# Kernel tuning notes

Hardware: AMD Instinct MI355X
Metric: run time of the kernel (lower is better)

## Reference

```python
import jax, jax.numpy as jnp
import numpy as np

N_PER_GRAPH = 32
DEGREE = 8
N_GRAPHS = 2048
IN_CH = 64
HID = 64
OUT = 4
EPS = 1e-5


def setup_inputs() -> dict:
    key = jax.random.key(0)
    ks = jax.random.split(key, 12)
    N = N_GRAPHS * N_PER_GRAPH
    # ring connectivity: node i -> (i+d) mod 32 within each graph, d=1..DEGREE
    i = np.arange(N_PER_GRAPH)
    offs = np.arange(1, DEGREE + 1)
    s = np.repeat(i, DEGREE)
    d = (s + np.tile(offs, N_PER_GRAPH)) % N_PER_GRAPH
    base = (np.arange(N_GRAPHS) * N_PER_GRAPH)[:, None]
    src = (base + s[None, :]).reshape(-1)
    dst = (base + d[None, :]).reshape(-1)
    edge_index = jnp.asarray(np.stack([src, dst]).astype(np.int32))
    batch = jnp.asarray((np.arange(N) // N_PER_GRAPH).astype(np.int32))

    def w(k, shape, fan_in):
        return jax.random.normal(k, shape, jnp.float32) / np.float32(np.sqrt(fan_in))

    return dict(
        x=jax.random.normal(ks[0], (N, IN_CH), jnp.float32),
        edge_weight=jax.random.uniform(ks[1], (edge_index.shape[1],), jnp.float32),
        W1a=w(ks[2], (IN_CH, HID), IN_CH), W1b=w(ks[3], (IN_CH, HID), IN_CH),
        b1=jnp.zeros((HID,), jnp.float32), g1=jnp.ones((HID,), jnp.float32), be1=jnp.zeros((HID,), jnp.float32),
        W2a=w(ks[4], (HID, 2 * HID), HID), W2b=w(ks[5], (HID, 2 * HID), HID),
        b2=jnp.zeros((2 * HID,), jnp.float32), g2=jnp.ones((2 * HID,), jnp.float32), be2=jnp.zeros((2 * HID,), jnp.float32),
        W3a=w(ks[6], (2 * HID, 2 * HID), 2 * HID), W3b=w(ks[7], (2 * HID, 2 * HID), 2 * HID),
        b3=jnp.zeros((2 * HID,), jnp.float32), g3=jnp.ones((2 * HID,), jnp.float32), be3=jnp.zeros((2 * HID,), jnp.float32),
        fcW=w(ks[8], (2 * HID, OUT), 2 * HID), fcb=jnp.zeros((OUT,), jnp.float32),
        edge_index=edge_index, batch=batch,
    )


def cheb_conv(x, src, dst, ew, W0, W1, b):
    # PyG ChebConv, K=2, sym normalization, lambda_max=2:
    # scaled Laplacian L_hat = L - I = -D^{-1/2} A D^{-1/2} (diag exactly 0)
    n = x.shape[0]
    deg = jnp.zeros((n,), x.dtype).at[src].add(ew)
    dinv = jnp.where(deg > 0, jax.lax.rsqrt(deg), 0.0)
    norm = -dinv[src] * ew * dinv[dst]
    tx1 = jnp.zeros_like(x).at[dst].add(norm[:, None] * x[src])  # [n, C] gather-scatter
    return x @ W0 + tx1 @ W1 + b


def batch_norm(x, g, b):
    # training-mode BatchNorm over the node dimension (biased variance, as torch)
    m = x.mean(0)
    v = x.var(0)
    return (x - m) * jax.lax.rsqrt(v + EPS) * g + b


def pool_half(x, src, dst, ew):
    # deterministic stand-in for graclus: pair consecutive nodes (pairs stay
    # within a graph since each graph has an even node count).
    n = x.shape[0]
    cluster = jnp.arange(n) // 2
    x2 = jax.ops.segment_max(x, cluster, num_segments=n // 2)
    s2, d2 = src // 2, dst // 2
    # zero-weight self loops == removing them (contribute 0 to degree & messages);
    # keeping duplicate edges == coalescing with sum under segment_sum ops.
    ew2 = jnp.where(s2 == d2, jnp.zeros_like(ew), ew)
    return x2, s2, d2, ew2


def forward(x, edge_weight, W1a, W1b, b1, g1, be1, W2a, W2b, b2, g2, be2,
            W3a, W3b, b3, g3, be3, fcW, fcb, edge_index, batch):
    src, dst = edge_index[0], edge_index[1]
    ew = edge_weight
    h = jax.nn.softplus(batch_norm(cheb_conv(x, src, dst, ew, W1a, W1b, b1), g1, be1))
    h, src, dst, ew = pool_half(h, src, dst, ew)
    h = jax.nn.softplus(batch_norm(cheb_conv(h, src, dst, ew, W2a, W2b, b2), g2, be2))
    h, src, dst, ew = pool_half(h, src, dst, ew)
    h = jax.nn.softplus(batch_norm(cheb_conv(h, src, dst, ew, W3a, W3b, b3), g3, be3))
    batch3 = batch[::4]  # batch vector after two halvings of consecutive pairs
    sums = jax.ops.segment_sum(h, batch3, num_segments=N_GRAPHS)
    cnt = jax.ops.segment_sum(jnp.ones((h.shape[0],), h.dtype), batch3, num_segments=N_GRAPHS)
    hg = sums / jnp.maximum(cnt, 1.0)[:, None]
    return jax.nn.log_softmax(hg @ fcW + fcb, axis=1)


def reference(x, edge_weight, W1a, W1b, b1, g1, be1, W2a, W2b, b2, g2, be2,
              W3a, W3b, b3, g3, be3, fcW, fcb, edge_index, batch):
    return forward(x, edge_weight, W1a, W1b, b1, g1, be1, W2a, W2b, b2, g2, be2,
                   W3a, W3b, b3, g3, be3, fcW, fcb, edge_index, batch)
```

## Files before the change

kernel.cpp:

```cpp
#include <hip/hip_runtime.h>

#define EPSV 1e-5f

typedef __attribute__((ext_vector_type(8))) short short8;
typedef __attribute__((ext_vector_type(4))) float f32x4;

__device__ __forceinline__ float softplus_f(float x){
    return fmaxf(x, 0.f) + log1pf(expf(-fabsf(x)));
}
__device__ __forceinline__ float bf2f(short u){
    union{unsigned int i; float f;} x; x.i = ((unsigned int)(unsigned short)u) << 16; return x.f;
}
__device__ __forceinline__ short f2bf(float f){
    union{float f; unsigned int i;} x; x.f = f;
    unsigned int r = x.i + 0x7fffu + ((x.i >> 16) & 1u);
    return (short)(r >> 16);
}

#define W1TA_OFF 0
#define W1TB_OFF 4608
#define W2TA_OFF 9216
#define W2TB_OFF 18432
#define W3TA_OFF 27648
#define W3TB_OFF 45056
#define WT_TOTAL 62464

__global__ void k_prep(const float* __restrict__ W1a, const float* __restrict__ W1b,
                       const float* __restrict__ W2a, const float* __restrict__ W2b,
                       const float* __restrict__ W3a, const float* __restrict__ W3b,
                       short* __restrict__ wt){
    int blk = blockIdx.x, tid = threadIdx.x;
    const float* src; short* dst; int N, SP, base;
    if      (blk < 16){  src = W1a; dst = wt + W1TA_OFF; N = 64;  SP = 72;  base = blk; }
    else if (blk < 32){  src = W1b; dst = wt + W1TB_OFF; N = 64;  SP = 72;  base = blk - 16; }
    else if (blk < 64){  src = W2a; dst = wt + W2TA_OFF; N = 128; SP = 72;  base = blk - 32; }
    else if (blk < 96){  src = W2b; dst = wt + W2TB_OFF; N = 128; SP = 72;  base = blk - 64; }
    else if (blk < 160){ src = W3a; dst = wt + W3TA_OFF; N = 128; SP = 136; base = blk - 96; }
    else              {  src = W3b; dst = wt + W3TB_OFF; N = 128; SP = 136; base = blk - 160; }
    int e = base * 256 + tid;
    int k = e / N, c = e % N;
    dst[c * SP + k] = f2bf(src[e]);
}

__global__ __launch_bounds__(256) void k_gat1(const float* __restrict__ x, const float* __restrict__ ew,
        short* __restrict__ xb1, short* __restrict__ tx1){
    __shared__ float ews[256], nrm[256], dinv[32];
    __shared__ __align__(16) short xsb[32][72];
    int g = blockIdx.x, tid = threadIdx.x;
    ews[tid] = ew[(size_t)g*256 + tid];
    {   const float4* xg = (const float4*)(x + (size_t)g*32*64);
        #pragma unroll
        for (int p = 0; p < 2; ++p){
            int i4 = tid + p*256;
            int r = i4 >> 4, cc = (i4 & 15)*4;
            float4 v = xg[i4];
            xsb[r][cc+0] = f2bf(v.x); xsb[r][cc+1] = f2bf(v.y);
            xsb[r][cc+2] = f2bf(v.z); xsb[r][cc+3] = f2bf(v.w);
        }
    }
    __syncthreads();
    if (tid < 32){
        float d = 0.f;
        #pragma unroll
        for (int k = 0; k < 8; ++k) d += ews[tid*8 + k];
        dinv[tid] = d > 0.f ? rsqrtf(d) : 0.f;
    }
    __syncthreads();
    {   int se = tid >> 3, de = (se + (tid & 7) + 1) & 31;
        nrm[tid] = -dinv[se] * ews[tid] * dinv[de]; }
    __syncthreads();
    int v = tid >> 3, ch = (tid & 7)*8;
    *(short8*)&xb1[((size_t)g*32 + v)*64 + ch] = *(const short8*)&xsb[v][ch];
    float acc[8];
    #pragma unroll
    for (int j = 0; j < 8; ++j) acc[j] = 0.f;
    #pragma unroll
    for (int k = 0; k < 8; ++k){
        int sl = (v - k - 1) & 31;
        float nw = nrm[sl*8 + k];
        short8 xv = *(const short8*)&xsb[sl][ch];
        #pragma unroll
        for (int j = 0; j < 8; ++j) acc[j] = fmaf(nw, bf2f(xv[j]), acc[j]);
    }
    short8 o;
    #pragma unroll
    for (int j = 0; j < 8; ++j) o[j] = f2bf(acc[j]);
    *(short8*)&tx1[((size_t)g*32 + v)*64 + ch] = o;
}

__global__ __launch_bounds__(256) void k_gat2(const short* __restrict__ h1, const float* __restrict__ ew,
        const float* __restrict__ scl1, const float* __restrict__ sft1,
        short* __restrict__ xb2, short* __restrict__ tx2){
    __shared__ float ews[256], nrm[256], dinv[16];
    __shared__ float scl[64], sft[64];
    __shared__ __align__(16) short xpb[16][72];
    int g = blockIdx.x, tid = threadIdx.x;
    ews[tid] = ew[(size_t)g*256 + tid];
    if (tid < 64){ scl[tid] = scl1[tid]; sft[tid] = sft1[tid]; }
    __syncthreads();
    if (tid < 128){
        int vo = tid >> 3, ch = (tid & 7)*8;
        short8 a = *(const short8*)&h1[((size_t)g*32 + 2*vo)*64 + ch];
        short8 b = *(const short8*)&h1[((size_t)g*32 + 2*vo + 1)*64 + ch];
        short8 o;
        #pragma unroll
        for (int j = 0; j < 8; ++j){
            float s = scl[ch+j], t = sft[ch+j];
            float va = softplus_f(bf2f(a[j])*s + t);
            float vb = softplus_f(bf2f(b[j])*s + t);
            o[j] = f2bf(fmaxf(va, vb));
        }
        *(short8*)&xpb[vo][ch] = o;
        *(short8*)&xb2[((size_t)g*16 + vo)*64 + ch] = o;
    }
    if (tid < 16){
        float d = 0.f;
        for (int t = tid*16; t < tid*16 + 16; ++t){
            int se = t >> 3, de = (se + (t & 7) + 1) & 31;
            float wv = ((se >> 1) == (de >> 1)) ? 0.f : ews[t];
            d += wv;
        }
        dinv[tid] = d > 0.f ? rsqrtf(d) : 0.f;
    }
    __syncthreads();
    {   int se = tid >> 3, de = (se + (tid & 7) + 1) & 31;
        float wv = ((se >> 1) == (de >> 1)) ? 0.f : ews[tid];
        nrm[tid] = -dinv[se >> 1] * wv * dinv[de >> 1]; }
    __syncthreads();
    if (tid < 128){
        int v = tid >> 3, ch = (tid & 7)*8;
        float acc[8];
        #pragma unroll
        for (int j = 0; j < 8; ++j) acc[j] = 0.f;
        #pragma unroll
        for (int dd = 0; dd < 2; ++dd){
            int d = v*2 + dd;
            #pragma unroll
            for (int k = 0; k < 8; ++k){
                int sl = (d - k - 1) & 31;
                float nw = nrm[sl*8 + k];
                short8 xv = *(const short8*)&xpb[sl >> 1][ch];
                #pragma unroll
                for (int j = 0; j < 8; ++j) acc[j] = fmaf(nw, bf2f(xv[j]), acc[j]);
            }
        }
        short8 o;
        #pragma unroll
        for (int j = 0; j < 8; ++j) o[j] = f2bf(acc[j]);
        *(short8*)&tx2[((size_t)g*16 + v)*64 + ch] = o;
    }
}

__global__ __launch_bounds__(256) void k_gat3(const short* __restrict__ h2, const float* __restrict__ ew,
        const float* __restrict__ scl2, const float* __restrict__ sft2,
        short* __restrict__ xb3, short* __restrict__ tx3){
    __shared__ float ews[256], nrm[256], dinv[8];
    __shared__ float scl[128], sft[128];
    __shared__ __align__(16) short xpb[8][136];
    int g = blockIdx.x, tid = threadIdx.x;
    ews[tid] = ew[(size_t)g*256 + tid];
    if (tid < 128){ scl[tid] = scl2[tid]; sft[tid] = sft2[tid]; }
    __syncthreads();
    if (tid < 128){
        int vo = tid >> 4, ch = (tid & 15)*8;
        short8 a = *(const short8*)&h2[((size_t)g*16 + 2*vo)*128 + ch];
        short8 b = *(const short8*)&h2[((size_t)g*16 + 2*vo + 1)*128 + ch];
        short8 o;
        #pragma unroll
        for (int j = 0; j < 8; ++j){
            float s = scl[ch+j], t = sft[ch+j];
            float va = softplus_f(bf2f(a[j])*s + t);
            float vb = softplus_f(bf2f(b[j])*s + t);
            o[j] = f2bf(fmaxf(va, vb));
        }
        *(short8*)&xpb[vo][ch] = o;
        *(short8*)&xb3[((size_t)g*8 + vo)*128 + ch] = o;
    }
    if (tid < 8){
        float d = 0.f;
        for (int t = tid*32; t < tid*32 + 32; ++t){
            int se = t >> 3, de = (se + (t & 7) + 1) & 31;
            float wv = ((se >> 2) == (de >> 2)) ? 0.f : ews[t];
            d += wv;
        }
        dinv[tid] = d > 0.f ? rsqrtf(d) : 0.f;
    }
    __syncthreads();
    {   int se = tid >> 3, de = (se + (tid & 7) + 1) & 31;
        float wv = ((se >> 2) == (de >> 2)) ? 0.f : ews[tid];
        nrm[tid] = -dinv[se >> 2] * wv * dinv[de >> 2]; }
    __syncthreads();
    if (tid < 128){
        int v = tid >> 4, ch = (tid & 15)*8;
        float acc[8];
        #pragma unroll
        for (int j = 0; j < 8; ++j) acc[j] = 0.f;
        #pragma unroll
        for (int dd = 0; dd < 4; ++dd){
            int d = v*4 + dd;
            #pragma unroll
            for (int k = 0; k < 8; ++k){
                int sl = (d - k - 1) & 31;
                float nw = nrm[sl*8 + k];
                short8 xv = *(const short8*)&xpb[sl >> 2][ch];
                #pragma unroll
                for (int j = 0; j < 8; ++j) acc[j] = fmaf(nw, bf2f(xv[j]), acc[j]);
            }
        }
        short8 o;
        #pragma unroll
        for (int j = 0; j < 8; ++j) o[j] = f2bf(acc[j]);
        *(short8*)&tx3[((size_t)g*8 + v)*128 + ch] = o;
    }
}

template<int BM, int CIN, int COUT, int NB>
__global__ __launch_bounds__(256) void k_gemm(const short* __restrict__ xb, const short* __restrict__ tx,
        const short* __restrict__ Wa, const short* __restrict__ Wb, int WSP,
        const float* __restrict__ bias, short* __restrict__ h, float* __restrict__ P){
    constexpr int RPW = BM/4, RT = RPW/16, CT = COUT/16, KC = CIN/64;
    __shared__ __align__(16) short As[BM][72];
    __shared__ __align__(16) short Bs[COUT][72];
    __shared__ float ssum[COUT], ssq[COUT];
    int blk = blockIdx.x, tid = threadIdx.x;
    int lane = tid & 63, w = tid >> 6, lrow = lane & 15, lk8 = lane >> 4;
    if (tid < COUT){ ssum[tid] = 0.f; ssq[tid] = 0.f; }
    f32x4 acc[RT][CT];
    #pragma unroll
    for (int rt = 0; rt < RT; ++rt)
        #pragma unroll
        for (int ct = 0; ct < CT; ++ct) acc[rt][ct] = (f32x4){0,0,0,0};

    #pragma unroll
    for (int seg = 0; seg < 2; ++seg){
        const short* Ag = seg ? tx : xb;
        const short* Wg = seg ? Wb : Wa;
        #pragma unroll
        for (int kc = 0; kc < KC; ++kc){
            __syncthreads();
            for (int idx = tid; idx < BM*8; idx += 256){
                int r = idx >> 3, ko = (idx & 7)*8;
                *(short8*)&As[r][ko] =
                    *(const short8*)&Ag[((size_t)(blk*BM + r))*CIN + kc*64 + ko];
            }
            for (int idx = tid; idx < COUT*8; idx += 256){
                int c = idx >> 3, ko = (idx & 7)*8;
                *(short8*)&Bs[c][ko] =
                    *(const short8*)&Wg[(size_t)c*WSP + kc*64 + ko];
            }
            __syncthreads();
            #pragma unroll
            for (int ks = 0; ks < 2; ++ks){
                short8 af[RT];
                #pragma unroll
                for (int rt = 0; rt < RT; ++rt)
                    af[rt] = *(const short8*)&As[w*RPW + rt*16 + lrow][ks*32 + lk8*8];
                #pragma unroll
                for (int ct = 0; ct < CT; ++ct){
                    short8 bf = *(const short8*)&Bs[ct*16 + lrow][ks*32 + lk8*8];
                    #pragma unroll
                    for (int rt = 0; rt < RT; ++rt)
                        acc[rt][ct] = __builtin_amdgcn_mfma_f32_16x16x32_bf16(af[rt], bf, acc[rt][ct], 0, 0, 0);
                }
            }
        }
    }
    #pragma unroll
    for (int ct = 0; ct < CT; ++ct){
        int col = ct*16 + lrow;
        float bb = bias[col];
        float s = 0.f, q = 0.f;
        #pragma unroll
        for (int rt = 0; rt < RT; ++rt){
            #pragma unroll
            for (int e = 0; e < 4; ++e){
                float v = acc[rt][ct][e] + bb;
                int row = blk*BM + w*RPW + rt*16 + lk8*4 + e;
                h[(size_t)row*COUT + col] = f2bf(v);
                s += v; q += v*v;
            }
        }
        s += __shfl_xor(s, 16); s += __shfl_xor(s, 32);
        q += __shfl_xor(q, 16); q += __shfl_xor(q, 32);
        if (lane < 16){ atomicAdd(&ssum[col], s); atomicAdd(&ssq[col], q); }
    }
    __syncthreads();
    if (tid < COUT){
        P[(size_t)tid*NB + blk]          = ssum[tid];
        P[(size_t)(COUT + tid)*NB + blk] = ssq[tid];
    }
}

template<int C, int NB>
__global__ void k_red(const float* __restrict__ P, const float* __restrict__ gamma,
                      const float* __restrict__ beta, float nl_inv,
                      float* __restrict__ scl, float* __restrict__ sft){
    __shared__ float r1[128], r2[128];
    int c = blockIdx.x, t = threadIdx.x;
    if (t < 128){
        float s = 0.f;
        for (int i = t; i < NB; i += 128) s += P[(size_t)c*NB + i];
        r1[t] = s;
    } else {
        float q = 0.f;
        for (int i = t - 128; i < NB; i += 128) q += P[(size_t)(C + c)*NB + i];
        r2[t - 128] = q;
    }
    __syncthreads();
    for (int s = 64; s > 0; s >>= 1){
        if (t < s) r1[t] += r1[t + s];
        else if (t >= 128 && t - 128 < s) r2[t - 128] += r2[t - 128 + s];
        __syncthreads();
    }
    if (t == 0){
        float m = r1[0] * nl_inv;
        float var = r2[0] * nl_inv - m*m;
        float rs = rsqrtf(var + EPSV) * gamma[c];
        scl[c] = rs;
        sft[c] = beta[c] - m*rs;
    }
}

__global__ __launch_bounds__(256) void k_head(const short* __restrict__ h3,
        const float* __restrict__ scl3, const float* __restrict__ sft3,
        const float* __restrict__ fcW, const float* __restrict__ fcb,
        float* __restrict__ out){
    int tid = threadIdx.x, w = tid >> 6, lane = tid & 63;
    int g = blockIdx.x*4 + w;
    int c0 = lane*2;
    float sc0 = scl3[c0], sh0 = sft3[c0];
    float sc1 = scl3[c0+1], sh1 = sft3[c0+1];
    float acc0 = 0.f, acc1 = 0.f;
    #pragma unroll
    for (int n = 0; n < 8; ++n){
        unsigned int v = *(const unsigned int*)&h3[((size_t)g*8 + n)*128 + c0];
        union{unsigned int i; float f;} lo, hi;
        lo.i = v << 16; hi.i = v & 0xffff0000u;
        acc0 += softplus_f(lo.f*sc0 + sh0);
        acc1 += softplus_f(hi.f*sc1 + sh1);
    }
    float hg0 = acc0 * 0.125f, hg1 = acc1 * 0.125f;
    float4 w0 = ((const float4*)fcW)[c0];
    float4 w1 = ((const float4*)fcW)[c0+1];
    float z0 = hg0*w0.x + hg1*w1.x;
    float z1 = hg0*w0.y + hg1*w1.y;
    float z2 = hg0*w0.z + hg1*w1.z;
    float z3 = hg0*w0.w + hg1*w1.w;
    #pragma unroll
    for (int d = 1; d < 64; d <<= 1){
        z0 += __shfl_xor(z0, d); z1 += __shfl_xor(z1, d);
        z2 += __shfl_xor(z2, d); z3 += __shfl_xor(z3, d);
    }
    if (lane == 0){
        z0 += fcb[0]; z1 += fcb[1]; z2 += fcb[2]; z3 += fcb[3];
        float mx = fmaxf(fmaxf(z0, z1), fmaxf(z2, z3));
        float lse = mx + logf(expf(z0-mx) + expf(z1-mx) + expf(z2-mx) + expf(z3-mx));
        *(float4*)(out + (size_t)g*4) = make_float4(z0-lse, z1-lse, z2-lse, z3-lse);
    }
}

extern "C" void kernel_launch(void* const* d_in, const int* in_sizes, int n_in,
                              void* d_out, int out_size, void* d_ws, size_t ws_size,
                              hipStream_t stream){
    const float* x   = (const float*)d_in[0];
    const float* ew  = (const float*)d_in[1];
    const float* W1a = (const float*)d_in[2];
    const float* W1b = (const float*)d_in[3];
    const float* b1  = (const float*)d_in[4];
    const float* g1  = (const float*)d_in[5];
    const float* be1 = (const float*)d_in[6];
    const float* W2a = (const float*)d_in[7];
    const float* W2b = (const float*)d_in[8];
    const float* b2  = (const float*)d_in[9];
    const float* g2  = (const float*)d_in[10];
    const float* be2 = (const float*)d_in[11];
    const float* W3a = (const float*)d_in[12];
    const float* W3b = (const float*)d_in[13];
    const float* b3  = (const float*)d_in[14];
    const float* g3  = (const float*)d_in[15];
    const float* be3 = (const float*)d_in[16];
    const float* fcW = (const float*)d_in[17];
    const float* fcb = (const float*)d_in[18];
    float* out = (float*)d_out;
    (void)in_sizes; (void)n_in; (void)out_size; (void)ws_size;

    short* xb1 = (short*)d_ws;
    short* tx1 = xb1 + (size_t)4194304;
    short* h1  = tx1 + (size_t)4194304;
    short* xb2 = h1  + (size_t)4194304;
    short* tx2 = xb2 + (size_t)2097152;
    short* h2  = tx2 + (size_t)2097152;
    short* xb3 = h2  + (size_t)4194304;
    short* tx3 = xb3 + (size_t)2097152;
    short* h3  = tx3 + (size_t)2097152;
    short* wT  = h3  + (size_t)2097152;
    float* fp  = (float*)(((uintptr_t)(wT + WT_TOTAL) + 255) & ~(uintptr_t)255);
    float* P1  = fp;
    float* P2  = P1 + 65536;
    float* P3  = P2 + 65536;
    float* scl1 = P3 + 65536;  float* sft1 = scl1 + 64;
    float* scl2 = sft1 + 64;   float* sft2 = scl2 + 128;
    float* scl3 = sft2 + 128;  float* sft3 = scl3 + 128;

    k_prep<<<224, 256, 0, stream>>>(W1a, W1b, W2a, W2b, W3a, W3b, wT);

    k_gat1<<<2048, 256, 0, stream>>>(x, ew, xb1, tx1);
    k_gemm<128,64,64,512><<<512, 256, 0, stream>>>(xb1, tx1, wT + W1TA_OFF, wT + W1TB_OFF, 72, b1, h1, P1);
    k_red<64,512><<<64, 256, 0, stream>>>(P1, g1, be1, 1.f/65536.f, scl1, sft1);

    k_gat2<<<2048, 256, 0, stream>>>(h1, ew, scl1, sft1, xb2, tx2);
    k_gemm<128,64,128,256><<<256, 256, 0, stream>>>(xb2, tx2, wT + W2TA_OFF, wT + W2TB_OFF, 72, b2, h2, P2);
    k_red<128,256><<<128, 256, 0, stream>>>(P2, g2, be2, 1.f/32768.f, scl2, sft2);

    k_gat3<<<2048, 256, 0, stream>>>(h2, ew, scl2, sft2, xb3, tx3);
    k_gemm<64,128,128,256><<<256, 256, 0, stream>>>(xb3, tx3, wT + W3TA_OFF, wT + W3TB_OFF, 136, b3, h3, P3);
    k_red<128,256><<<128, 256, 0, stream>>>(P3, g3, be3, 1.f/16384.f, scl3, sft3);

    k_head<<<512, 256, 0, stream>>>(h3, scl3, sft3, fcW, fcb, out);
}
```

Measured before the change: 214.7 us.

## Fuse gather, GEMM and batch-norm stat reduction into one kernel per layer

Each ChebConv layer's gather/pool kernel, MFMA GEMM and stat-reduction kernel are merged into a single kernel. The x and Tx tiles stay in LDS instead of round-tripping through global memory. Batch-norm statistics go into global atomics, and the last block to finish (tracked by a counter) computes scale and shift, so the separate reduction and weight-prep launches go away. In exchange, every block re-converts and transposes the weights into LDS, LDS use per block goes up (which may lower occupancy), and the float atomic sums make the result order nondeterministic.

Result: slower. 271.0 us (+26.2%).

```diff
diff --git a/kernel.cpp b/kernel.cpp
--- a/kernel.cpp
+++ b/kernel.cpp
@@ -17,266 +17,101 @@
     return (short)(r >> 16);
 }
 
-#define W1TA_OFF 0
-#define W1TB_OFF 4608
-#define W2TA_OFF 9216
-#define W2TB_OFF 18432
-#define W3TA_OFF 27648
-#define W3TB_OFF 45056
-#define WT_TOTAL 62464
-
-__global__ void k_prep(const float* __restrict__ W1a, const float* __restrict__ W1b,
-                       const float* __restrict__ W2a, const float* __restrict__ W2b,
-                       const float* __restrict__ W3a, const float* __restrict__ W3b,
-                       short* __restrict__ wt){
+__global__ __launch_bounds__(256) void k_l1(const float* __restrict__ x, const float* __restrict__ ew,
+        const float* __restrict__ W1a, const float* __restrict__ W1b, const float* __restrict__ b1,
+        const float* __restrict__ g1, const float* __restrict__ be1,
+        short* __restrict__ h1, float* __restrict__ gs, float* __restrict__ gq,
+        int* __restrict__ cnt, float* __restrict__ scl1, float* __restrict__ sft1){
+    __shared__ __align__(16) short A[128][72], T[128][72], Ba[64][72], Bb[64][72];
+    __shared__ float ews[256], nrm[256], dinv[32], ssum[64], ssq[64];
+    __shared__ int isLast;
     int blk = blockIdx.x, tid = threadIdx.x;
-    const float* src; short* dst; int N, SP, base;
-    if      (blk < 16){  src = W1a; dst = wt + W1TA_OFF; N = 64;  SP = 72;  base = blk; }
-    else if (blk < 32){  src = W1b; dst = wt + W1TB_OFF; N = 64;  SP = 72;  base = blk - 16; }
-    else if (blk < 64){  src = W2a; dst = wt + W2TA_OFF; N = 128; SP = 72;  base = blk - 32; }
-    else if (blk < 96){  src = W2b; dst = wt + W2TB_OFF; N = 128; SP = 72;  base = blk - 64; }
-    else if (blk < 160){ src = W3a; dst = wt + W3TA_OFF; N = 128; SP = 136; base = blk - 96; }
-    else              {  src = W3b; dst = wt + W3TB_OFF; N = 128; SP = 136; base = blk - 160; }
-    int e = base * 256 + tid;
-    int k = e / N, c = e % N;
-    dst[c * SP + k] = f2bf(src[e]);
-}
-
-__global__ __launch_bounds__(256) void k_gat1(const float* __restrict__ x, const float* __restrict__ ew,
-        short* __restrict__ xb1, short* __restrict__ tx1){
-    __shared__ float ews[256], nrm[256], dinv[32];
-    __shared__ __align__(16) short xsb[32][72];
-    int g = blockIdx.x, tid = threadIdx.x;
-    ews[tid] = ew[(size_t)g*256 + tid];
-    {   const float4* xg = (const float4*)(x + (size_t)g*32*64);
-        #pragma unroll
-        for (int p = 0; p < 2; ++p){
-            int i4 = tid + p*256;
+    if (tid < 64){ ssum[tid] = 0.f; ssq[tid] = 0.f; }
+    for (int idx = tid; idx < 4096; idx += 256){
+        int k = idx >> 6, c = idx & 63;
+        Ba[c][k] = f2bf(W1a[idx]);
+        Bb[c][k] = f2bf(W1b[idx]);
+    }
+    for (int gi = 0; gi < 4; ++gi){
+        int g = blk*4 + gi;
+        ews[tid] = ew[(size_t)g*256 + tid];
+        const float4* xg = (const float4*)(x + (size_t)g*2048);
+        #pragma unroll
+        for (int q2 = 0; q2 < 2; ++q2){
+            int i4 = tid + q2*256;
             int r = i4 >> 4, cc = (i4 & 15)*4;
             float4 v = xg[i4];
-            xsb[r][cc+0] = f2bf(v.x); xsb[r][cc+1] = f2bf(v.y);
-            xsb[r][cc+2] = f2bf(v.z); xsb[r][cc+3] = f2bf(v.w);
-        }
-    }
-    __syncthreads();
-    if (tid < 32){
-        float d = 0.f;
-        #pragma unroll
-        for (int k = 0; k < 8; ++k) d += ews[tid*8 + k];
-        dinv[tid] = d > 0.f ? rsqrtf(d) : 0.f;
-    }
-    __syncthreads();
-    {   int se = tid >> 3, de = (se + (tid & 7) + 1) & 31;
-        nrm[tid] = -dinv[se] * ews[tid] * dinv[de]; }
-    __syncthreads();
-    int v = tid >> 3, ch = (tid & 7)*8;
-    *(short8*)&xb1[((size_t)g*32 + v)*64 + ch] = *(const short8*)&xsb[v][ch];
-    float acc[8];
-    #pragma unroll
-    for (int j = 0; j < 8; ++j) acc[j] = 0.f;
-    #pragma unroll
-    for (int k = 0; k < 8; ++k){
-        int sl = (v - k - 1) & 31;
-        float nw = nrm[sl*8 + k];
-        short8 xv = *(const short8*)&xsb[sl][ch];
-        #pragma unroll
-        for (int j = 0; j < 8; ++j) acc[j] = fmaf(nw, bf2f(xv[j]), acc[j]);
-    }
-    short8 o;
-    #pragma unroll
-    for (int j = 0; j < 8; ++j) o[j] = f2bf(acc[j]);
-    *(short8*)&tx1[((size_t)g*32 + v)*64 + ch] = o;
-}
-
-__global__ __launch_bounds__(256) void k_gat2(const short* __restrict__ h1, const float* __restrict__ ew,
-        const float* __restrict__ scl1, const float* __restrict__ sft1,
-        short* __restrict__ xb2, short* __restrict__ tx2){
-    __shared__ float ews[256], nrm[256], dinv[16];
-    __shared__ float scl[64], sft[64];
-    __shared__ __align__(16) short xpb[16][72];
-    int g = blockIdx.x, tid = threadIdx.x;
-    ews[tid] = ew[(size_t)g*256 + tid];
-    if (tid < 64){ scl[tid] = scl1[tid]; sft[tid] = sft1[tid]; }
-    __syncthreads();
-    if (tid < 128){
-        int vo = tid >> 3, ch = (tid & 7)*8;
-        short8 a = *(const short8*)&h1[((size_t)g*32 + 2*vo)*64 + ch];
-        short8 b = *(const short8*)&h1[((size_t)g*32 + 2*vo + 1)*64 + ch];
-        short8 o;
-        #pragma unroll
-        for (int j = 0; j < 8; ++j){
-            float s = scl[ch+j], t = sft[ch+j];
-            float va = softplus_f(bf2f(a[j])*s + t);
-            float vb = softplus_f(bf2f(b[j])*s + t);
-            o[j] = f2bf(fmaxf(va, vb));
-        }
-        *(short8*)&xpb[vo][ch] = o;
-        *(short8*)&xb2[((size_t)g*16 + vo)*64 + ch] = o;
-    }
-    if (tid < 16){
-        float d = 0.f;
-        for (int t = tid*16; t < tid*16 + 16; ++t){
-            int se = t >> 3, de = (se + (t & 7) + 1) & 31;
-            float wv = ((se >> 1) == (de >> 1)) ? 0.f : ews[t];
-            d += wv;
-        }
-        dinv[tid] = d > 0.f ? rsqrtf(d) : 0.f;
-    }
-    __syncthreads();
-    {   int se = tid >> 3, de = (se + (tid & 7) + 1) & 31;
-        float wv = ((se >> 1) == (de >> 1)) ? 0.f : ews[tid];
-        nrm[tid] = -dinv[se >> 1] * wv * dinv[de >> 1]; }
-    __syncthreads();
-    if (tid < 128){
-        int v = tid >> 3, ch = (tid & 7)*8;
-        float acc[8];
-        #pragma unroll
-        for (int j = 0; j < 8; ++j) acc[j] = 0.f;
-        #pragma unroll
-        for (int dd = 0; dd < 2; ++dd){
-            int d = v*2 + dd;
+            A[gi*32+r][cc+0] = f2bf(v.x); A[gi*32+r][cc+1] = f2bf(v.y);
+            A[gi*32+r][cc+2] = f2bf(v.z); A[gi*32+r][cc+3] = f2bf(v.w);
+        }
+        __syncthreads();
+        if (tid < 32){
+            float d = 0.f;
+            #pragma unroll
+            for (int k = 0; k < 8; ++k) d += ews[tid*8 + k];
+            dinv[tid] = d > 0.f ? rsqrtf(d) : 0.f;
+        }
+        __syncthreads();
+        {   int se = tid >> 3, de = (se + (tid & 7) + 1) & 31;
+            nrm[tid] = -dinv[se] * ews[tid] * dinv[de]; }
+        __syncthreads();
+        {   int v = tid >> 3, ch = (tid & 7)*8;
+            float acc[8];
+            #pragma unroll
+            for (int j = 0; j < 8; ++j) acc[j] = 0.f;
             #pragma unroll
             for (int k = 0; k < 8; ++k){
-                int sl = (d - k - 1) & 31;
+                int sl = (v - k - 1) & 31;
                 float nw = nrm[sl*8 + k];
-                short8 xv = *(const short8*)&xpb[sl >> 1][ch];
+                short8 xv = *(const short8*)&A[gi*32 + sl][ch];
                 #pragma unroll
                 for (int j = 0; j < 8; ++j) acc[j] = fmaf(nw, bf2f(xv[j]), acc[j]);
             }
-        }
-        short8 o;
-        #pragma unroll
-        for (int j = 0; j < 8; ++j) o[j] = f2bf(acc[j]);
-        *(short8*)&tx2[((size_t)g*16 + v)*64 + ch] = o;
-    }
-}
-
-__global__ __launch_bounds__(256) void k_gat3(const short* __restrict__ h2, const float* __restrict__ ew,
-        const float* __restrict__ scl2, const float* __restrict__ sft2,
-        short* __restrict__ xb3, short* __restrict__ tx3){
-    __shared__ float ews[256], nrm[256], dinv[8];
-    __shared__ float scl[128], sft[128];
-    __shared__ __align__(16) short xpb[8][136];
-    int g = blockIdx.x, tid = threadIdx.x;
-    ews[tid] = ew[(size_t)g*256 + tid];
-    if (tid < 128){ scl[tid] = scl2[tid]; sft[tid] = sft2[tid]; }
-    __syncthreads();
-    if (tid < 128){
-        int vo = tid >> 4, ch = (tid & 15)*8;
-        short8 a = *(const short8*)&h2[((size_t)g*16 + 2*vo)*128 + ch];
-        short8 b = *(const short8*)&h2[((size_t)g*16 + 2*vo + 1)*128 + ch];
-        short8 o;
-        #pragma unroll
-        for (int j = 0; j < 8; ++j){
-            float s = scl[ch+j], t = sft[ch+j];
-            float va = softplus_f(bf2f(a[j])*s + t);
-            float vb = softplus_f(bf2f(b[j])*s + t);
-            o[j] = f2bf(fmaxf(va, vb));
-        }
-        *(short8*)&xpb[vo][ch] = o;
-        *(short8*)&xb3[((size_t)g*8 + vo)*128 + ch] = o;
-    }
-    if (tid < 8){
-        float d = 0.f;
-        for (int t = tid*32; t < tid*32 + 32; ++t){
-            int se = t >> 3, de = (se + (t & 7) + 1) & 31;
-            float wv = ((se >> 2) == (de >> 2)) ? 0.f : ews[t];
-            d += wv;
-        }
-        dinv[tid] = d > 0.f ? rsqrtf(d) : 0.f;
-    }
-    __syncthreads();
-    {   int se = tid >> 3, de = (se + (tid & 7) + 1) & 31;
-        float wv = ((se >> 2) == (de >> 2)) ? 0.f : ews[tid];
-        nrm[tid] = -dinv[se >> 2] * wv * dinv[de >> 2]; }
-    __syncthreads();
-    if (tid < 128){
-        int v = tid >> 4, ch = (tid & 15)*8;
-        float acc[8];
-        #pragma unroll
-        for (int j = 0; j < 8; ++j) acc[j] = 0.f;
-        #pragma unroll
-        for (int dd = 0; dd < 4; ++dd){
-            int d = v*4 + dd;
-            #pragma unroll
-            for (int k = 0; k < 8; ++k){
-                int sl = (d - k - 1) & 31;
-                float nw = nrm[sl*8 + k];
-                short8 xv = *(const short8*)&xpb[sl >> 2][ch];
+            short8 o;
+            #pragma unroll
+            for (int j = 0; j < 8; ++j) o[j] = f2bf(acc[j]);
+            *(short8*)&T[gi*32 + v][ch] = o;
+        }
+        __syncthreads();
+    }
+    int lane = tid & 63, w = tid >> 6, lrow = lane & 15, lk8 = lane >> 4;
+    f32x4 acc[2][4];
+    #pragma unroll
+    for (int rt = 0; rt < 2; ++rt)
+        #pragma unroll
+        for (int ct = 0; ct < 4; ++ct) acc[rt][ct] = (f32x4){0,0,0,0};
+    typedef short row72[72];
+    #pragma unroll
+    for (int seg = 0; seg < 2; ++seg){
+        row72* Ag = seg ? T : A;
+        row72* Bg = seg ? Bb : Ba;
+        #pragma unroll
+        for (int ks = 0; ks < 2; ++ks){
+            short8 af[2];
+            #pragma unroll
+            for (int rt = 0; rt < 2; ++rt)
+                af[rt] = *(const short8*)&Ag[w*32 + rt*16 + lrow][ks*32 + lk8*8];
+            #pragma unroll
+            for (int ct = 0; ct < 4; ++ct){
+                short8 bf = *(const short8*)&Bg[ct*16 + lrow][ks*32 + lk8*8];
                 #pragma unroll
-                for (int j = 0; j < 8; ++j) acc[j] = fmaf(nw, bf2f(xv[j]), acc[j]);
-            }
-        }
-        short8 o;
-        #pragma unroll
-        for (int j = 0; j < 8; ++j) o[j] = f2bf(acc[j]);
-        *(short8*)&tx3[((size_t)g*8 + v)*128 + ch] = o;
-    }
-}
-
-template<int BM, int CIN, int COUT, int NB>
-__global__ __launch_bounds__(256) void k_gemm(const short* __restrict__ xb, const short* __restrict__ tx,
-        const short* __restrict__ Wa, const short* __restrict__ Wb, int WSP,
-        const float* __restrict__ bias, short* __restrict__ h, float* __restrict__ P){
-    constexpr int RPW = BM/4, RT = RPW/16, CT = COUT/16, KC = CIN/64;
-    __shared__ __align__(16) short As[BM][72];
-    __shared__ __align__(16) short Bs[COUT][72];
-    __shared__ float ssum[COUT], ssq[COUT];
-    int blk = blockIdx.x, tid = threadIdx.x;
-    int lane = tid & 63, w = tid >> 6, lrow = lane & 15, lk8 = lane >> 4;
-    if (tid < COUT){ ssum[tid] = 0.f; ssq[tid] = 0.f; }
-    f32x4 acc[RT][CT];
-    #pragma unroll
-    for (int rt = 0; rt < RT; ++rt)
-        #pragma unroll
-        for (int ct = 0; ct < CT; ++ct) acc[rt][ct] = (f32x4){0,0,0,0};
-
-    #pragma unroll
-    for (int seg = 0; seg < 2; ++seg){
-        const short* Ag = seg ? tx : xb;
-        const short* Wg = seg ? Wb : Wa;
-        #pragma unroll
-        for (int kc = 0; kc < KC; ++kc){
-            __syncthreads();
-            for (int idx = tid; idx < BM*8; idx += 256){
-                int r = idx >> 3, ko = (idx & 7)*8;
-                *(short8*)&As[r][ko] =
-                    *(const short8*)&Ag[((size_t)(blk*BM + r))*CIN + kc*64 + ko];
-            }
-            for (int idx = tid; idx < COUT*8; idx += 256){
-                int c = idx >> 3, ko = (idx & 7)*8;
-                *(short8*)&Bs[c][ko] =
-                    *(const short8*)&Wg[(size_t)c*WSP + kc*64 + ko];
-            }
-            __syncthreads();
-            #pragma unroll
-            for (int ks = 0; ks < 2; ++ks){
-                short8 af[RT];
-                #pragma unroll
-                for (int rt = 0; rt < RT; ++rt)
-                    af[rt] = *(const short8*)&As[w*RPW + rt*16 + lrow][ks*32 + lk8*8];
-                #pragma unroll
-                for (int ct = 0; ct < CT; ++ct){
-                    short8 bf = *(const short8*)&Bs[ct*16 + lrow][ks*32 + lk8*8];
-                    #pragma unroll
-                    for (int rt = 0; rt < RT; ++rt)
-                        acc[rt][ct] = __builtin_amdgcn_mfma_f32_16x16x32_bf16(af[rt], bf, acc[rt][ct], 0, 0, 0);
-                }
-            }
-        }
-    }
-    #pragma unroll
-    for (int ct = 0; ct < CT; ++ct){
+                for (int rt = 0; rt < 2; ++rt)
+                    acc[rt][ct] = __builtin_amdgcn_mfma_f32_16x16x32_bf16(af[rt], bf, acc[rt][ct], 0, 0, 0);
+            }
+        }
+    }
+    #pragma unroll
+    for (int ct = 0; ct < 4; ++ct){
         int col = ct*16 + lrow;
-        float bb = bias[col];
+        float bb = b1[col];
         float s = 0.f, q = 0.f;
         #pragma unroll
-        for (int rt = 0; rt < RT; ++rt){
+        for (int rt = 0; rt < 2; ++rt){
             #pragma unroll
             for (int e = 0; e < 4; ++e){
                 float v = acc[rt][ct][e] + bb;
-                int row = blk*BM + w*RPW + rt*16 + lk8*4 + e;
-                h[(size_t)row*COUT + col] = f2bf(v);
+                int row = blk*128 + w*32 + rt*16 + lk8*4 + e;
+                h1[(size_t)row*64 + col] = f2bf(v);
                 s += v; q += v*v;
             }
         }
@@ -285,39 +120,269 @@
         if (lane < 16){ atomicAdd(&ssum[col], s); atomicAdd(&ssq[col], q); }
     }
     __syncthreads();
-    if (tid < COUT){
-        P[(size_t)tid*NB + blk]          = ssum[tid];
-        P[(size_t)(COUT + tid)*NB + blk] = ssq[tid];
-    }
-}
-
-template<int C, int NB>
-__global__ void k_red(const float* __restrict__ P, const float* __restrict__ gamma,
-                      const float* __restrict__ beta, float nl_inv,
-                      float* __restrict__ scl, float* __restrict__ sft){
-    __shared__ float r1[128], r2[128];
-    int c = blockIdx.x, t = threadIdx.x;
-    if (t < 128){
-        float s = 0.f;
-        for (int i = t; i < NB; i += 128) s += P[(size_t)c*NB + i];
-        r1[t] = s;
-    } else {
-        float q = 0.f;
-        for (int i = t - 128; i < NB; i += 128) q += P[(size_t)(C + c)*NB + i];
-        r2[t - 128] = q;
-    }
-    __syncthreads();
-    for (int s = 64; s > 0; s >>= 1){
-        if (t < s) r1[t] += r1[t + s];
-        else if (t >= 128 && t - 128 < s) r2[t - 128] += r2[t - 128 + s];
-        __syncthreads();
-    }
-    if (t == 0){
-        float m = r1[0] * nl_inv;
-        float var = r2[0] * nl_inv - m*m;
-        float rs = rsqrtf(var + EPSV) * gamma[c];
-        scl[c] = rs;
-        sft[c] = beta[c] - m*rs;
+    if (tid < 64){ atomicAdd(&gs[tid], ssum[tid]); atomicAdd(&gq[tid], ssq[tid]); }
+    __syncthreads();
+    if (tid == 0) isLast = (atomicAdd(cnt, 1) == 511);
+    __syncthreads();
+    if (isLast && tid < 64){
+        float s = atomicAdd(&gs[tid], 0.f);
+        float q = atomicAdd(&gq[tid], 0.f);
+        float m = s * (1.f/65536.f);
+        float var = q * (1.f/65536.f) - m*m;
+        float rs = rsqrtf(var + EPSV) * g1[tid];
+        scl1[tid] = rs; sft1[tid] = be1[tid] - m*rs;
+    }
+}
+
+__global__ __launch_bounds__(256) void k_l2(const short* __restrict__ h1, const float* __restrict__ ew,
+        const float* __restrict__ scl1, const float* __restrict__ sft1,
+        const float* __restrict__ W2a, const float* __restrict__ W2b, const float* __restrict__ b2,
+        const float* __restrict__ g2, const float* __restrict__ be2,
+        short* __restrict__ h2, float* __restrict__ gs, float* __restrict__ gq,
+        int* __restrict__ cnt, float* __restrict__ scl2, float* __restrict__ sft2){
+    __shared__ __align__(16) short A[64][72], T[64][72], Ba[128][72], Bb[128][72];
+    __shared__ float ews[256], nrm[256], dinv[16], sscl[64], ssft[64], ssum[128], ssq[128];
+    __shared__ int isLast;
+    int blk = blockIdx.x, tid = threadIdx.x;
+    if (tid < 128){ ssum[tid] = 0.f; ssq[tid] = 0.f; }
+    if (tid < 64){ sscl[tid] = scl1[tid]; ssft[tid] = sft1[tid]; }
+    for (int idx = tid; idx < 8192; idx += 256){
+        int k = idx >> 7, c = idx & 127;
+        Ba[c][k] = f2bf(W2a[idx]);
+        Bb[c][k] = f2bf(W2b[idx]);
+    }
+    __syncthreads();
+    for (int gi = 0; gi < 4; ++gi){
+        int g = blk*4 + gi;
+        ews[tid] = ew[(size_t)g*256 + tid];
+        __syncthreads();
+        if (tid < 128){
+            int vo = tid >> 3, ch = (tid & 7)*8;
+            short8 a = *(const short8*)&h1[((size_t)g*32 + 2*vo)*64 + ch];
+            short8 b = *(const short8*)&h1[((size_t)g*32 + 2*vo + 1)*64 + ch];
+            short8 o;
+            #pragma unroll
+            for (int j = 0; j < 8; ++j){
+                float s = sscl[ch+j], t = ssft[ch+j];
+                float va = softplus_f(bf2f(a[j])*s + t);
+                float vb = softplus_f(bf2f(b[j])*s + t);
+                o[j] = f2bf(fmaxf(va, vb));
+            }
+            *(short8*)&A[gi*16 + vo][ch] = o;
+        }
+        if (tid < 16){
+            float d = 0.f;
+            for (int t = tid*16; t < tid*16 + 16; ++t){
+                int se = t >> 3, de = (se + (t & 7) + 1) & 31;
+                float wv = ((se >> 1) == (de >> 1)) ? 0.f : ews[t];
+                d += wv;
+            }
+            dinv[tid] = d > 0.f ? rsqrtf(d) : 0.f;
+        }
+        __syncthreads();
+        {   int se = tid >> 3, de = (se + (tid & 7) + 1) & 31;
+            float wv = ((se >> 1) == (de >> 1)) ? 0.f : ews[tid];
+            nrm[tid] = -dinv[se >> 1] * wv * dinv[de >> 1]; }
+        __syncthreads();
+        if (tid < 128){
+            int v = tid >> 3, ch = (tid & 7)*8;
+            float acc[8];
+            #pragma unroll
+            for (int j = 0; j < 8; ++j) acc[j] = 0.f;
+            #pragma unroll
+            for (int dd = 0; dd < 2; ++dd){
+                int d = v*2 + dd;
+                #pragma unroll
+                for (int k = 0; k < 8; ++k){
+                    int sl = (d - k - 1) & 31;
+                    float nw = nrm[sl*8 + k];
+                    short8 xv = *(const short8*)&A[gi*16 + (sl >> 1)][ch];
+                    #pragma unroll
+                    for (int j = 0; j < 8; ++j) acc[j] = fmaf(nw, bf2f(xv[j]), acc[j]);
+                }
+            }
+            short8 o;
+            #pragma unroll
+            for (int j = 0; j < 8; ++j) o[j] = f2bf(acc[j]);
+            *(short8*)&T[gi*16 + v][ch] = o;
+        }
+        __syncthreads();
+    }
+    int lane = tid & 63, w = tid >> 6, lrow = lane & 15, lk8 = lane >> 4;
+    f32x4 acc[8];
+    #pragma unroll
+    for (int ct = 0; ct < 8; ++ct) acc[ct] = (f32x4){0,0,0,0};
+    typedef short row72[72];
+    #pragma unroll
+    for (int seg = 0; seg < 2; ++seg){
+        row72* Ag = seg ? T : A;
+        row72* Bg = seg ? Bb : Ba;
+        #pragma unroll
+        for (int ks = 0; ks < 2; ++ks){
+            short8 af = *(const short8*)&Ag[w*16 + lrow][ks*32 + lk8*8];
+            #pragma unroll
+            for (int ct = 0; ct < 8; ++ct){
+                short8 bf = *(const short8*)&Bg[ct*16 + lrow][ks*32 + lk8*8];
+                acc[ct] = __builtin_amdgcn_mfma_f32_16x16x32_bf16(af, bf, acc[ct], 0, 0, 0);
+            }
+        }
+    }
+    #pragma unroll
+    for (int ct = 0; ct < 8; ++ct){
+        int col = ct*16 + lrow;
+        float bb = b2[col];
+        float s = 0.f, q = 0.f;
+        #pragma unroll
+        for (int e = 0; e < 4; ++e){
+            float v = acc[ct][e] + bb;
+            int row = blk*64 + w*16 + lk8*4 + e;
+            h2[(size_t)row*128 + col] = f2bf(v);
+            s += v; q += v*v;
+        }
+        s += __shfl_xor(s, 16); s += __shfl_xor(s, 32);
+        q += __shfl_xor(q, 16); q += __shfl_xor(q, 32);
+        if (lane < 16){ atomicAdd(&ssum[col], s); atomicAdd(&ssq[col], q); }
+    }
+    __syncthreads();
+    if (tid < 128){ atomicAdd(&gs[tid], ssum[tid]); atomicAdd(&gq[tid], ssq[tid]); }
+    __syncthreads();
+    if (tid == 0) isLast = (atomicAdd(cnt, 1) == 511);
+    __syncthreads();
+    if (isLast && tid < 128){
+        float s = atomicAdd(&gs[tid], 0.f);
+        float q = atomicAdd(&gq[tid], 0.f);
+        float m = s * (1.f/32768.f);
+        float var = q * (1.f/32768.f) - m*m;
+        float rs = rsqrtf(var + EPSV) * g2[tid];
+        scl2[tid] = rs; sft2[tid] = be2[tid] - m*rs;
+    }
+}
+
+__global__ __launch_bounds__(256) void k_l3(const short* __restrict__ h2, const float* __restrict__ ew,
+        const float* __restrict__ scl2, const float* __restrict__ sft2,
+        const float* __restrict__ W3a, const float* __restrict__ W3b, const float* __restrict__ b3,
+        const float* __restrict__ g3, const float* __restrict__ be3,
+        short* __restrict__ h3, float* __restrict__ gs, float* __restrict__ gq,
+        int* __restrict__ cnt, float* __restrict__ scl3, float* __restrict__ sft3){
+    __shared__ __align__(16) short A[64][136], T[64][136], Ba[64][136], Bb[64][136];
+    __shared__ float ews[256], nrm[256], dinv[8], sscl[128], ssft[128], ssum[128], ssq[128];
+    __shared__ int isLast;
+    int blk = blockIdx.x, tid = threadIdx.x;
+    if (tid < 128){ ssum[tid] = 0.f; ssq[tid] = 0.f; sscl[tid] = scl2[tid]; ssft[tid] = sft2[tid]; }
+    __syncthreads();
+    for (int gi = 0; gi < 8; ++gi){
+        int g = blk*8 + gi;
+        ews[tid] = ew[(size_t)g*256 + tid];
+        __syncthreads();
+        if (tid < 128){
+            int vo = tid >> 4, ch = (tid & 15)*8;
+            short8 a = *(const short8*)&h2[((size_t)g*16 + 2*vo)*128 + ch];
+            short8 b = *(const short8*)&h2[((size_t)g*16 + 2*vo + 1)*128 + ch];
+            short8 o;
+            #pragma unroll
+            for (int j = 0; j < 8; ++j){
+                float s = sscl[ch+j], t = ssft[ch+j];
+                float va = softplus_f(bf2f(a[j])*s + t);
+                float vb = softplus_f(bf2f(b[j])*s + t);
+                o[j] = f2bf(fmaxf(va, vb));
+            }
+            *(short8*)&A[gi*8 + vo][ch] = o;
+        }
+        if (tid < 8){
+            float d = 0.f;
+            for (int t = tid*32; t < tid*32 + 32; ++t){
+                int se = t >> 3, de = (se + (t & 7) + 1) & 31;
+                float wv = ((se >> 2) == (de >> 2)) ? 0.f : ews[t];
+                d += wv;
+            }
+            dinv[tid] = d > 0.f ? rsqrtf(d) : 0.f;
+        }
+        __syncthreads();
+        {   int se = tid >> 3, de = (se + (tid & 7) + 1) & 31;
+            float wv = ((se >> 2) == (de >> 2)) ? 0.f : ews[tid];
+            nrm[tid] = -dinv[se >> 2] * wv * dinv[de >> 2]; }
+        __syncthreads();
+        if (tid < 128){
+            int v = tid >> 4, ch = (tid & 15)*8;
+            float acc[8];
+            #pragma unroll
+            for (int j = 0; j < 8; ++j) acc[j] = 0.f;
+            #pragma unroll
+            for (int dd = 0; dd < 4; ++dd){
+                int d = v*4 + dd;
+                #pragma unroll
+                for (int k = 0; k < 8; ++k){
+                    int sl = (d - k - 1) & 31;
+                    float nw = nrm[sl*8 + k];
+                    short8 xv = *(const short8*)&A[gi*8 + (sl >> 2)][ch];
+                    #pragma unroll
+                    for (int j = 0; j < 8; ++j) acc[j] = fmaf(nw, bf2f(xv[j]), acc[j]);
+                }
+            }
+            short8 o;
+            #pragma unroll
+            for (int j = 0; j < 8; ++j) o[j] = f2bf(acc[j]);
+            *(short8*)&T[gi*8 + v][ch] = o;
+        }
+        __syncthreads();
+    }
+    int lane = tid & 63, w = tid >> 6, lrow = lane & 15, lk8 = lane >> 4;
+    typedef short row136[136];
+    #pragma unroll
+    for (int cc = 0; cc < 2; ++cc){
+        __syncthreads();
+        for (int idx = tid; idx < 8192; idx += 256){
+            int k = idx >> 6, c = idx & 63;
+            Ba[c][k] = f2bf(W3a[(size_t)k*128 + cc*64 + c]);
+            Bb[c][k] = f2bf(W3b[(size_t)k*128 + cc*64 + c]);
+        }
+        __syncthreads();
+        f32x4 acc[4];
+        #pragma unroll
+        for (int ct = 0; ct < 4; ++ct) acc[ct] = (f32x4){0,0,0,0};
+        #pragma unroll
+        for (int seg = 0; seg < 2; ++seg){
+            row136* Ag = seg ? T : A;
+            row136* Bg = seg ? Bb : Ba;
+            #pragma unroll
+            for (int ks = 0; ks < 4; ++ks){
+                short8 af = *(const short8*)&Ag[w*16 + lrow][ks*32 + lk8*8];
+                #pragma unroll
+                for (int ct = 0; ct < 4; ++ct){
+                    short8 bf = *(const short8*)&Bg[ct*16 + lrow][ks*32 + lk8*8];
+                    acc[ct] = __builtin_amdgcn_mfma_f32_16x16x32_bf16(af, bf, acc[ct], 0, 0, 0);
+                }
+            }
+        }
+        #pragma unroll
+        for (int ct = 0; ct < 4; ++ct){
+            int col = cc*64 + ct*16 + lrow;
+            float bb = b3[col];
+            float s = 0.f, q = 0.f;
+            #pragma unroll
+            for (int e = 0; e < 4; ++e){
+                float v = acc[ct][e] + bb;
+                int row = blk*64 + w*16 + lk8*4 + e;
+                h3[(size_t)row*128 + col] = f2bf(v);
+                s += v; q += v*v;
+            }
+            s += __shfl_xor(s, 16); s += __shfl_xor(s, 32);
+            q += __shfl_xor(q, 16); q += __shfl_xor(q, 32);
+            if (lane < 16){ atomicAdd(&ssum[col], s); atomicAdd(&ssq[col], q); }
+        }
+    }
+    __syncthreads();
+    if (tid < 128){ atomicAdd(&gs[tid], ssum[tid]); atomicAdd(&gq[tid], ssq[tid]); }
+    __syncthreads();
+    if (tid == 0) isLast = (atomicAdd(cnt, 1) == 255);
+    __syncthreads();
+    if (isLast && tid < 128){
+        float s = atomicAdd(&gs[tid], 0.f);
+        float q = atomicAdd(&gq[tid], 0.f);
+        float m = s * (1.f/16384.f);
+        float var = q * (1.f/16384.f) - m*m;
+        float rs = rsqrtf(var + EPSV) * g3[tid];
+        scl3[tid] = rs; sft3[tid] = be3[tid] - m*rs;
     }
 }
 
@@ -384,37 +449,27 @@
     float* out = (float*)d_out;
     (void)in_sizes; (void)n_in; (void)out_size; (void)ws_size;
 
-    short* xb1 = (short*)d_ws;
-    short* tx1 = xb1 + (size_t)4194304;
-    short* h1  = tx1 + (size_t)4194304;
-    short* xb2 = h1  + (size_t)4194304;
-    short* tx2 = xb2 + (size_t)2097152;
-    short* h2  = tx2 + (size_t)2097152;
-    short* xb3 = h2  + (size_t)4194304;
-    short* tx3 = xb3 + (size_t)2097152;
-    short* h3  = tx3 + (size_t)2097152;
-    short* wT  = h3  + (size_t)2097152;
-    float* fp  = (float*)(((uintptr_t)(wT + WT_TOTAL) + 255) & ~(uintptr_t)255);
-    float* P1  = fp;
-    float* P2  = P1 + 65536;
-    float* P3  = P2 + 65536;
-    float* scl1 = P3 + 65536;  float* sft1 = scl1 + 64;
-    float* scl2 = sft1 + 64;   float* sft2 = scl2 + 128;
-    float* scl3 = sft2 + 128;  float* sft3 = scl3 + 128;
-
-    k_prep<<<224, 256, 0, stream>>>(W1a, W1b, W2a, W2b, W3a, W3b, wT);
-
-    k_gat1<<<2048, 256, 0, stream>>>(x, ew, xb1, tx1);
-    k_gemm<128,64,64,512><<<512, 256, 0, stream>>>(xb1, tx1, wT + W1TA_OFF, wT + W1TB_OFF, 72, b1, h1, P1);
-    k_red<64,512><<<64, 256, 0, stream>>>(P1, g1, be1, 1.f/65536.f, scl1, sft1);
-
-    k_gat2<<<2048, 256, 0, stream>>>(h1, ew, scl1, sft1, xb2, tx2);
-    k_gemm<128,64,128,256><<<256, 256, 0, stream>>>(xb2, tx2, wT + W2TA_OFF, wT + W2TB_OFF, 72, b2, h2, P2);
-    k_red<128,256><<<128, 256, 0, stream>>>(P2, g2, be2, 1.f/32768.f, scl2, sft2);
-
-    k_gat3<<<2048, 256, 0, stream>>>(h2, ew, scl2, sft2, xb3, tx3);
-    k_gemm<64,128,128,256><<<256, 256, 0, stream>>>(xb3, tx3, wT + W3TA_OFF, wT + W3TB_OFF, 136, b3, h3, P3);
-    k_red<128,256><<<128, 256, 0, stream>>>(P3, g3, be3, 1.f/16384.f, scl3, sft3);
-
+    short* h1 = (short*)d_ws;
+    short* h2 = h1 + (size_t)4194304;
+    short* h3 = h2 + (size_t)4194304;
+    float* fp = (float*)(((uintptr_t)(h3 + 2097152) + 255) & ~(uintptr_t)255);
+    int*   cnt1 = (int*)(fp + 0);
+    int*   cnt2 = (int*)(fp + 1);
+    int*   cnt3 = (int*)(fp + 2);
+    float* gs1 = fp + 4;    float* gq1 = fp + 68;
+    float* gs2 = fp + 132;  float* gq2 = fp + 260;
+    float* gs3 = fp + 388;  float* gq3 = fp + 516;
+    float* scl1 = fp + 644; float* sft1 = fp + 708;
+    float* scl2 = fp + 772; float* sft2 = fp + 900;
+    float* scl3 = fp + 1028; float* sft3 = fp + 1156;
+
+    hipMemsetAsync(fp, 0, 644*sizeof(float), stream);
+
+    k_l1<<<512, 256, 0, stream>>>(x, ew, W1a, W1b, b1, g1, be1,
+                                  h1, gs1, gq1, cnt1, scl1, sft1);
+    k_l2<<<512, 256, 0, stream>>>(h1, ew, scl1, sft1, W2a, W2b, b2, g2, be2,
+                                  h2, gs2, gq2, cnt2, scl2, sft2);
+    k_l3<<<256, 256, 0, stream>>>(h2, ew, scl2, sft2, W3a, W3b, b3, g3, be3,
+                                  h3, gs3, gq3, cnt3, scl3, sft3);
     k_head<<<512, 256, 0, stream>>>(h3, scl3, sft3, fcW, fcb, out);
 }
```
